# Kernel tuning notes

Measured on AMD Instinct MI355X. Metric: run time of the kernel, lower is better.

## Reference

```python
import jax, jax.numpy as jnp
import numpy as np

B, S, HID = 2, 2048, 3072
NH, NKV, HD = 16, 8, 256
N_REP = NH // NKV
BITS, BLK = 4, 128
THETA = 10000.0
NEG = -1e9


def quantize_bfp(x, bits=BITS, block_size=BLK):
    """Block-floating-point quantization: blocks of `block_size` along the last
    (head_dim) axis share one power-of-two exponent; mantissas get `bits` levels
    (sign + bits-1), round-to-nearest."""
    shape = x.shape
    xb = x.reshape(-1, block_size)
    maxabs = jnp.max(jnp.abs(xb), axis=-1, keepdims=True)
    e = jnp.floor(jnp.log2(jnp.maximum(maxabs, 1e-30)))
    scale = jnp.exp2(e - (bits - 2))  # largest mantissa ~ 2^(bits-1)-1 covers maxabs
    qmax = 2.0 ** (bits - 1) - 1.0
    q = jnp.clip(jnp.round(xb / scale), -qmax, qmax) * scale
    q = jnp.where(maxabs > 0, q, 0.0)
    return q.reshape(shape)


def rotate_half(x):
    x1, x2 = jnp.split(x, 2, axis=-1)
    return jnp.concatenate((-x2, x1), axis=-1)


def setup_inputs() -> dict:
    key = jax.random.key(0)
    ks = jax.random.split(key, 5)
    hidden_states = jax.random.normal(ks[0], (B, S, HID), dtype=jnp.float32)
    sd = 0.02
    Wq = jax.random.normal(ks[1], (NH * HD, HID), dtype=jnp.float32) * sd
    Wk = jax.random.normal(ks[2], (NKV * HD, HID), dtype=jnp.float32) * sd
    Wv = jax.random.normal(ks[3], (NKV * HD, HID), dtype=jnp.float32) * sd
    Wo = jax.random.normal(ks[4], (HID, NH * HD), dtype=jnp.float32) * sd
    # rotary tables (HF convention: concat(freqs, freqs))
    pos = jnp.arange(S, dtype=jnp.float32)
    inv_freq = 1.0 / (THETA ** (jnp.arange(0, HD, 2, dtype=jnp.float32) / HD))
    freqs = jnp.einsum('s,d->sd', pos, inv_freq)
    emb = jnp.concatenate((freqs, freqs), axis=-1)  # (S, HD)
    cos = jnp.cos(emb)[None]  # (1, S, HD)
    sin = jnp.sin(emb)[None]
    # additive causal mask (B, 1, S, S)
    causal = jnp.where(jnp.tril(jnp.ones((S, S), dtype=bool)), 0.0, NEG).astype(jnp.float32)
    attention_mask = jnp.broadcast_to(causal[None, None], (B, 1, S, S))
    return {"hidden_states": hidden_states, "Wq": Wq, "Wk": Wk, "Wv": Wv,
            "Wo": Wo, "cos": cos, "sin": sin, "attention_mask": attention_mask}


def reference(hidden_states, Wq, Wk, Wv, Wo, cos, sin, attention_mask):
    b, s, _ = hidden_states.shape
    q = jnp.einsum('bsh,dh->bsd', hidden_states, Wq).reshape(b, s, NH, HD).transpose(0, 2, 1, 3)
    k = jnp.einsum('bsh,dh->bsd', hidden_states, Wk).reshape(b, s, NKV, HD).transpose(0, 2, 1, 3)
    v = jnp.einsum('bsh,dh->bsd', hidden_states, Wv).reshape(b, s, NKV, HD).transpose(0, 2, 1, 3)
    # RoPE (cos/sin unsqueezed at dim 1 -> (1,1,S,HD))
    c, sn = cos[:, None], sin[:, None]
    q = q * c + rotate_half(q) * sn
    k = k * c + rotate_half(k) * sn
    # int4 BFP quantization of keys (along rows of head_dim)
    k = quantize_bfp(k)
    # GQA: repeat kv heads
    k = jnp.repeat(k, N_REP, axis=1)
    v = jnp.repeat(v, N_REP, axis=1)
    scores = jnp.einsum('bhqd,bhkd->bhqk', q, k) / jnp.sqrt(jnp.float32(HD))
    scores = scores + attention_mask
    attn = jax.nn.softmax(scores.astype(jnp.float32), axis=-1).astype(q.dtype)
    out = jnp.einsum('bhqk,bhkd->bhqd', attn, v)
    out = out.transpose(0, 2, 1, 3).reshape(b, s, NH * HD)
    return jnp.einsum('bsd,hd->bsh', out, Wo)
```

## Files before the change

kernel.cpp:

```cpp
#include <hip/hip_runtime.h>
#include <math.h>

#define Bsz 2
#define Ssz 2048
#define HIDs 3072
#define NHs 16
#define NKVs 8
#define HDs 256

typedef _Float16 f16;
typedef _Float16 f16x8 __attribute__((ext_vector_type(8)));
typedef _Float16 f16x4 __attribute__((ext_vector_type(4)));
typedef float f32x4 __attribute__((ext_vector_type(4)));

__device__ __forceinline__ void async16(const f16* g, f16* l) {
    __builtin_amdgcn_global_load_lds(
        (const __attribute__((address_space(1))) void*)g,
        (__attribute__((address_space(3))) void*)l, 16, 0, 0);
}

__device__ __forceinline__ float row_max16(float v) {
    int t;
    t = __builtin_amdgcn_mov_dpp(__float_as_int(v), 0x121, 0xf, 0xf, false);
    v = fmaxf(v, __int_as_float(t));
    t = __builtin_amdgcn_mov_dpp(__float_as_int(v), 0x122, 0xf, 0xf, false);
    v = fmaxf(v, __int_as_float(t));
    t = __builtin_amdgcn_mov_dpp(__float_as_int(v), 0x124, 0xf, 0xf, false);
    v = fmaxf(v, __int_as_float(t));
    t = __builtin_amdgcn_mov_dpp(__float_as_int(v), 0x128, 0xf, 0xf, false);
    v = fmaxf(v, __int_as_float(t));
    return v;
}
__device__ __forceinline__ float row_sum16(float v) {
    int t;
    t = __builtin_amdgcn_mov_dpp(__float_as_int(v), 0x121, 0xf, 0xf, false);
    v = v + __int_as_float(t);
    t = __builtin_amdgcn_mov_dpp(__float_as_int(v), 0x122, 0xf, 0xf, false);
    v = v + __int_as_float(t);
    t = __builtin_amdgcn_mov_dpp(__float_as_int(v), 0x124, 0xf, 0xf, false);
    v = v + __int_as_float(t);
    t = __builtin_amdgcn_mov_dpp(__float_as_int(v), 0x128, 0xf, 0xf, false);
    v = v + __int_as_float(t);
    return v;
}

#define N4_HS  3145728
#define N4_WQ  3145728
#define N4_WK  1572864
#define N4_WV  1572864
#define N4_WO  3145728
#define N4_TOT (N4_HS + N4_WQ + N4_WK + N4_WV + N4_WO)

__global__ void cast_all_kernel(const float4* __restrict__ hs, const float4* __restrict__ wq,
                                const float4* __restrict__ wk, const float4* __restrict__ wv,
                                const float4* __restrict__ wo,
                                f16x4* __restrict__ hs_h, f16x4* __restrict__ wq_h,
                                f16x4* __restrict__ wk_h, f16x4* __restrict__ wv_h,
                                f16x4* __restrict__ wo_h) {
    int i = blockIdx.x * blockDim.x + threadIdx.x;
    const float4* src; f16x4* dst; int off;
    if (i < N4_HS)                       { src = hs; dst = hs_h; off = i; }
    else if (i < N4_HS + N4_WQ)          { src = wq; dst = wq_h; off = i - N4_HS; }
    else if (i < N4_HS + N4_WQ + N4_WK)  { src = wk; dst = wk_h; off = i - (N4_HS + N4_WQ); }
    else if (i < N4_TOT - N4_WO)         { src = wv; dst = wv_h; off = i - (N4_HS + N4_WQ + N4_WK); }
    else                                 { src = wo; dst = wo_h; off = i - (N4_TOT - N4_WO); }
    float4 v = src[off];
    f16x4 r;
    r[0] = (f16)v.x; r[1] = (f16)v.y; r[2] = (f16)v.z; r[3] = (f16)v.w;
    dst[off] = r;
}

__global__ __launch_bounds__(256) void gemm_nt_f16(
    const f16* __restrict__ A, const f16* __restrict__ Bm, float* __restrict__ C,
    int M, int N, int K)
{
    __shared__ __align__(16) f16 As[128 * 32];
    __shared__ __align__(16) f16 Bs[128 * 32];
    const int tid  = threadIdx.x;
    const int wave = tid >> 6, lane = tid & 63;
    const int l15  = lane & 15, quad = lane >> 4;
    const int m0 = blockIdx.y * 128, n0 = blockIdx.x * 128;
    const int wm = (wave >> 1) * 64, wn = (wave & 1) * 64;
    const int srow = wave * 32 + (lane >> 2);
    const int scol = (lane & 3) * 8;

    f32x4 acc[4][4];
    const f32x4 fz = {0.f, 0.f, 0.f, 0.f};
#pragma unroll
    for (int i = 0; i < 4; i++)
#pragma unroll
        for (int j = 0; j < 4; j++) acc[i][j] = fz;

    const f16* Ag0 = A  + (size_t)(m0 + srow) * K + scol;
    const f16* Ag1 = A  + (size_t)(m0 + srow + 16) * K + scol;
    const f16* Bg0 = Bm + (size_t)(n0 + srow) * K + scol;
    const f16* Bg1 = Bm + (size_t)(n0 + srow + 16) * K + scol;
    f16* Al0 = As + (wave * 32) * 32;
    f16* Al1 = As + (wave * 32 + 16) * 32;
    f16* Bl0 = Bs + (wave * 32) * 32;
    f16* Bl1 = Bs + (wave * 32 + 16) * 32;

    for (int k0 = 0; k0 < K; k0 += 32) {
        __syncthreads();
        async16(Ag0 + k0, Al0);
        async16(Ag1 + k0, Al1);
        async16(Bg0 + k0, Bl0);
        async16(Bg1 + k0, Bl1);
        __syncthreads();
        f16x8 af[4], bfr[4];
#pragma unroll
        for (int i = 0; i < 4; i++)
            af[i] = *(const f16x8*)(As + (wm + i * 16 + l15) * 32 + quad * 8);
#pragma unroll
        for (int j = 0; j < 4; j++)
            bfr[j] = *(const f16x8*)(Bs + (wn + j * 16 + l15) * 32 + quad * 8);
#pragma unroll
        for (int i = 0; i < 4; i++)
#pragma unroll
            for (int j = 0; j < 4; j++)
                acc[i][j] = __builtin_amdgcn_mfma_f32_16x16x32_f16(af[i], bfr[j], acc[i][j], 0, 0, 0);
    }
#pragma unroll
    for (int i = 0; i < 4; i++) {
        const int r = m0 + wm + i * 16 + quad * 4;
#pragma unroll
        for (int j = 0; j < 4; j++) {
            const int c = n0 + wn + j * 16 + l15;
#pragma unroll
            for (int rr = 0; rr < 4; rr++)
                C[(size_t)(r + rr) * N + c] = acc[i][j][rr];
        }
    }
}

__global__ void rope_q_kernel(const float* __restrict__ qp, const float* __restrict__ cosb,
                              const float* __restrict__ sinb, f16* __restrict__ qo) {
    const int s = blockIdx.x, h = blockIdx.y, b = blockIdx.z;
    const int d = threadIdx.x;
    const float* row = qp + (size_t)(b * Ssz + s) * (NHs * HDs) + h * HDs;
    float x = row[d];
    float other = (d < 128) ? -row[d + 128] : row[d - 128];
    float val = (x * cosb[s * HDs + d] + other * sinb[s * HDs + d]) * 0.0625f;
    qo[((size_t)(b * NHs + h) * Ssz + s) * HDs + d] = (f16)val;
}

__global__ void rope_quant_k_kernel(const float* __restrict__ kp, const float* __restrict__ cosb,
                                    const float* __restrict__ sinb, f16* __restrict__ ko) {
    const int s = blockIdx.x, h = blockIdx.y, b = blockIdx.z;
    const int d = threadIdx.x;
    const float* row = kp + (size_t)(b * Ssz + s) * (NKVs * HDs) + h * HDs;
    float x = row[d];
    float other = (d < 128) ? -row[d + 128] : row[d - 128];
    float val = x * cosb[s * HDs + d] + other * sinb[s * HDs + d];
    __shared__ float red[256];
    red[d] = fabsf(val);
    __syncthreads();
    for (int off = 64; off >= 1; off >>= 1) {
        if ((d & 127) < off) red[d] = fmaxf(red[d], red[d + off]);
        __syncthreads();
    }
    float maxabs = red[d & 128];
    float out;
    if (maxabs > 0.f) {
        int ex;
        frexpf(maxabs, &ex);
        float scale = ldexpf(1.0f, ex - 3);
        float q = rintf(val / scale);
        q = fminf(7.f, fmaxf(-7.f, q));
        out = q * scale;
    } else out = 0.f;
    ko[((size_t)(b * NKVs + h) * Ssz + s) * HDs + d] = (f16)out;
}

__global__ __launch_bounds__(256) void transpose_v_kernel(
    const float* __restrict__ proj, f16* __restrict__ vt)
{
    const int s0 = blockIdx.x * 64, c0 = blockIdx.y * 64, b = blockIdx.z;
    const int tid = threadIdx.x;
    __shared__ f16 T[64 * 72];
    {
        const int r = tid >> 2, cc = (tid & 3) * 16;
        const float* src = proj + (size_t)(b * Ssz + s0 + r) * (NKVs * HDs) + c0 + cc;
        f16 tmp[16];
#pragma unroll
        for (int q4 = 0; q4 < 4; q4++) {
            float4 v = *(const float4*)(src + q4 * 4);
            tmp[q4 * 4 + 0] = (f16)v.x; tmp[q4 * 4 + 1] = (f16)v.y;
            tmp[q4 * 4 + 2] = (f16)v.z; tmp[q4 * 4 + 3] = (f16)v.w;
        }
        *(f16x8*)(T + r * 72 + cc)     = *(f16x8*)(tmp);
        *(f16x8*)(T + r * 72 + cc + 8) = *(f16x8*)(tmp + 8);
    }
    __syncthreads();
    {
        const int d = tid >> 2, sc = (tid & 3) * 16;
        f16 tmp[16];
#pragma unroll
        for (int j = 0; j < 16; j++) tmp[j] = T[(sc + j) * 72 + d];
        const int col = c0 + d;
        const int kh = col >> 8, dd = col & 255;
        f16* dst = vt + ((size_t)(b * NKVs + kh) * HDs + dd) * Ssz + s0 + sc;
        *(f16x8*)(dst)     = *(f16x8*)(tmp);
        *(f16x8*)(dst + 8) = *(f16x8*)(tmp + 8);
    }
}

__global__ __launch_bounds__(256, 2) void attn_kernel(
    const f16* __restrict__ Q,
    const f16* __restrict__ Kq,
    const f16* __restrict__ Vt,
    f16* __restrict__ O)
{
    const int qt = (gridDim.x - 1) - blockIdx.x;
    const int h = blockIdx.y, b = blockIdx.z;
    const int kh = h >> 1;
    const int tid = threadIdx.x;
    const int wave = tid >> 6, lane = tid & 63;
    const int l15 = lane & 15, quad = lane >> 4;
    const int wrow = qt * 128 + wave * 32;

    const f16* Qb  = Q  + ((size_t)(b * NHs  + h)  * Ssz) * HDs;
    const f16* Kg  = Kq + ((size_t)(b * NKVs + kh) * Ssz) * HDs;
    const f16* Vtg = Vt + ((size_t)(b * NKVs + kh) * HDs) * Ssz;

    __shared__ __align__(16) f16 Ks[2][32 * 256];
    __shared__ __align__(16) f16 Vs[2][256 * 32];
    __shared__ __align__(16) f16 Pl[4 * 32 * 40];
    f16* Pw = Pl + wave * 32 * 40;

    const int k_r  = lane >> 5;
    const int k_c  = lane & 31;
    const int v_r  = lane >> 2;
    const int v_gc = (lane & 3) ^ ((v_r >> 1) & 3);

    auto stage = [&](int kt2, int bb) {
        const int kvb_ = kt2 * 32;
#pragma unroll
        for (int t = 0; t < 4; t++) {
            const int r2 = wave * 8 + t * 2;
            const int gc = k_c ^ ((2 * t + k_r) & 7);
            async16(Kg + (size_t)(kvb_ + r2 + k_r) * 256 + gc * 8, &Ks[bb][r2 * 256]);
        }
#pragma unroll
        for (int t = 0; t < 4; t++) {
            const int d0 = wave * 64 + t * 16;
            async16(Vtg + (size_t)(d0 + v_r) * Ssz + kvb_ + v_gc * 8, &Vs[bb][d0 * 32]);
        }
    };

    f16x8 qf0[8], qf1[8];
    {
        const f16* qrow0 = Qb + (size_t)(wrow + l15) * HDs + quad * 8;
        const f16* qrow1 = qrow0 + (size_t)16 * HDs;
#pragma unroll
        for (int ks = 0; ks < 8; ks++) {
            qf0[ks] = *(const f16x8*)(qrow0 + ks * 32);
            qf1[ks] = *(const f16x8*)(qrow1 + ks * 32);
        }
    }

    const f32x4 fz = {0.f, 0.f, 0.f, 0.f};
    f32x4 accO0[16], accO1[16];
#pragma unroll
    for (int jn = 0; jn < 16; jn++) { accO0[jn] = fz; accO1[jn] = fz; }
    float mrow0[4], mrow1[4], lp0[4], lp1[4];
#pragma unroll
    for (int r = 0; r < 4; r++) { mrow0[r] = -1e30f; mrow1[r] = -1e30f; lp0[r] = 0.f; lp1[r] = 0.f; }

    const int nk = 4 * qt + 4;
    const int wave_max_row = wrow + 31;
    const int kswz = l15 & 7;
    const int vswz = (l15 >> 1) & 3;

    stage(0, 0);
    __syncthreads();

    for (int kt = 0; kt < nk; kt++) {
        const int kvb = kt * 32;
        const int cur = kt & 1;
        if (kt + 1 < nk) stage(kt + 1, cur ^ 1);
        const f16* Ksc = Ks[cur];
        const f16* Vsc = Vs[cur];

        if (kvb <= wave_max_row) {
            f32x4 s00 = fz, s01 = fz, s10 = fz, s11 = fz;
#pragma unroll
            for (int ks = 0; ks < 8; ks++) {
                const int cpos = ((ks * 4 + quad) ^ kswz) * 8;
                f16x8 kf0 = *(const f16x8*)(Ksc + l15 * 256 + cpos);
                f16x8 kf1 = *(const f16x8*)(Ksc + (16 + l15) * 256 + cpos);
                s00 = __builtin_amdgcn_mfma_f32_16x16x32_f16(qf0[ks], kf0, s00, 0, 0, 0);
                s01 = __builtin_amdgcn_mfma_f32_16x16x32_f16(qf0[ks], kf1, s01, 0, 0, 0);
                s10 = __builtin_amdgcn_mfma_f32_16x16x32_f16(qf1[ks], kf0, s10, 0, 0, 0);
                s11 = __builtin_amdgcn_mfma_f32_16x16x32_f16(qf1[ks], kf1, s11, 0, 0, 0);
            }
            float a0[4], a1[4];
            bool need = false;
            const bool diag = (kvb + 31 > wrow);
#pragma unroll
            for (int r = 0; r < 4; r++) {
                float x0 = s00[r], x1 = s01[r];
                const int row0 = wrow + quad * 4 + r;
                if (diag) {
                    if (kvb + l15 > row0)      x0 = -1e30f;
                    if (kvb + 16 + l15 > row0) x1 = -1e30f;
                }
                float rmax = row_max16(fmaxf(x0, x1));
                float mold = mrow0[r];
                bool upd = rmax > mold + 8.f;
                float mnew = upd ? rmax : mold;
                a0[r] = upd ? __expf(mold - rmax) : 1.0f;
                need = need || upd;
                float p0 = __expf(x0 - mnew);
                float p1 = __expf(x1 - mnew);
                lp0[r] = lp0[r] * a0[r] + (p0 + p1);
                mrow0[r] = mnew;
                Pw[(quad * 4 + r) * 40 + l15]      = (f16)p0;
                Pw[(quad * 4 + r) * 40 + 16 + l15] = (f16)p1;
                float y0 = s10[r], y1 = s11[r];
                const int row1 = row0 + 16;
                if (diag) {
                    if (kvb + l15 > row1)      y0 = -1e30f;
                    if (kvb + 16 + l15 > row1) y1 = -1e30f;
                }
                float rmax1 = row_max16(fmaxf(y0, y1));
                float mold1 = mrow1[r];
                bool upd1 = rmax1 > mold1 + 8.f;
                float mnew1 = upd1 ? rmax1 : mold1;
                a1[r] = upd1 ? __expf(mold1 - rmax1) : 1.0f;
                need = need || upd1;
                float q0 = __expf(y0 - mnew1);
                float q1 = __expf(y1 - mnew1);
                lp1[r] = lp1[r] * a1[r] + (q0 + q1);
                mrow1[r] = mnew1;
                Pw[(16 + quad * 4 + r) * 40 + l15]      = (f16)q0;
                Pw[(16 + quad * 4 + r) * 40 + 16 + l15] = (f16)q1;
            }
            if (__any(need)) {
#pragma unroll
                for (int jn = 0; jn < 16; jn++) {
                    f32x4 t0 = accO0[jn], t1 = accO1[jn];
                    t0[0] *= a0[0]; t0[1] *= a0[1]; t0[2] *= a0[2]; t0[3] *= a0[3];
                    t1[0] *= a1[0]; t1[1] *= a1[1]; t1[2] *= a1[2]; t1[3] *= a1[3];
                    accO0[jn] = t0; accO1[jn] = t1;
                }
            }
            f16x8 pf0 = *(const f16x8*)(Pw + l15 * 40 + quad * 8);
            f16x8 pf1 = *(const f16x8*)(Pw + (16 + l15) * 40 + quad * 8);
#pragma unroll
            for (int jn = 0; jn < 16; jn++) {
                f16x8 vf = *(const f16x8*)(Vsc + (jn * 16 + l15) * 32 + (quad ^ vswz) * 8);
                accO0[jn] = __builtin_amdgcn_mfma_f32_16x16x32_f16(pf0, vf, accO0[jn], 0, 0, 0);
                accO1[jn] = __builtin_amdgcn_mfma_f32_16x16x32_f16(pf1, vf, accO1[jn], 0, 0, 0);
            }
        }
        __syncthreads();
    }
#pragma unroll
    for (int r = 0; r < 4; r++) {
        const int row0 = wrow + quad * 4 + r;
        const float inv0 = 1.0f / row_sum16(lp0[r]);
        f16* orow0 = O + ((size_t)(b * Ssz) + row0) * (NHs * HDs) + h * HDs;
#pragma unroll
        for (int jn = 0; jn < 16; jn++)
            orow0[jn * 16 + l15] = (f16)(accO0[jn][r] * inv0);
        const int row1 = row0 + 16;
        const float inv1 = 1.0f / row_sum16(lp1[r]);
        f16* orow1 = O + ((size_t)(b * Ssz) + row1) * (NHs * HDs) + h * HDs;
#pragma unroll
        for (int jn = 0; jn < 16; jn++)
            orow1[jn * 16 + l15] = (f16)(accO1[jn][r] * inv1);
    }
}

extern "C" void kernel_launch(void* const* d_in, const int* in_sizes, int n_in,
                              void* d_out, int out_size, void* d_ws, size_t ws_size,
                              hipStream_t stream) {
    const float* hs   = (const float*)d_in[0];
    const float* Wq   = (const float*)d_in[1];
    const float* Wk   = (const float*)d_in[2];
    const float* Wv   = (const float*)d_in[3];
    const float* Wo   = (const float*)d_in[4];
    const float* cosb = (const float*)d_in[5];
    const float* sinb = (const float*)d_in[6];
    float* out = (float*)d_out;

    char* ws = (char*)d_ws;
    f16*   hs_h = (f16*)(ws);
    f16*   wo_h = (f16*)(ws + 25165824);
    float* proj = (float*)(ws + 50331648);
    f16*   q_h  = (f16*)(ws + 117440512);
    f16*   k_h  = (f16*)(ws + 150994944);
    f16*   vt_h = (f16*)(ws + 167772160);
    f16*   ao_h = (f16*)proj;

    cast_all_kernel<<<N4_TOT / 256, 256, 0, stream>>>(
        (const float4*)hs, (const float4*)Wq, (const float4*)Wk,
        (const float4*)Wv, (const float4*)Wo,
        (f16x4*)hs_h, (f16x4*)q_h, (f16x4*)k_h, (f16x4*)vt_h, (f16x4*)wo_h);

    gemm_nt_f16<<<dim3(4096 / 128, 4096 / 128), 256, 0, stream>>>(hs_h, q_h, proj, 4096, 4096, 3072);
    rope_q_kernel<<<dim3(Ssz, NHs, Bsz), 256, 0, stream>>>(proj, cosb, sinb, q_h);
    gemm_nt_f16<<<dim3(2048 / 128, 4096 / 128), 256, 0, stream>>>(hs_h, k_h, proj, 4096, 2048, 3072);
    rope_quant_k_kernel<<<dim3(Ssz, NKVs, Bsz), 256, 0, stream>>>(proj, cosb, sinb, k_h);
    gemm_nt_f16<<<dim3(2048 / 128, 4096 / 128), 256, 0, stream>>>(hs_h, vt_h, proj, 4096, 2048, 3072);
    transpose_v_kernel<<<dim3(Ssz / 64, (NKVs * HDs) / 64, Bsz), 256, 0, stream>>>(proj, vt_h);
    attn_kernel<<<dim3(Ssz / 128, NHs, Bsz), 256, 0, stream>>>(q_h, k_h, vt_h, ao_h);
    gemm_nt_f16<<<dim3(3072 / 128, 4096 / 128), 256, 0, stream>>>(ao_h, wo_h, out, 4096, 3072, 4096);
}
```

Before: 1.085 ms.

## Remap attention blocks to XCDs for KV-head L2 locality and single-buffer K/V

Block indices are remapped so that all query tiles sharing one (batch, KV head) pair land on the same XCD, with causal tiles ordered to balance load, aiming to improve L2 reuse of K and V. The double-buffered K/V LDS staging is also replaced by a single buffer loaded synchronously each iteration. This halves LDS use, which may allow more blocks per CU, but it exposes global-load latency because loads no longer overlap compute. The remapping hard-codes the grid shape (16x16x2).

```diff
diff --git a/kernel.cpp b/kernel.cpp
--- a/kernel.cpp
+++ b/kernel.cpp
@@ -211,9 +211,18 @@
     const f16* __restrict__ Vt,
     f16* __restrict__ O)
 {
-    const int qt = (gridDim.x - 1) - blockIdx.x;
-    const int h = blockIdx.y, b = blockIdx.z;
-    const int kh = h >> 1;
+    const int flat = blockIdx.x + (blockIdx.y << 4) + (blockIdx.z << 8);
+    const int xcd  = flat & 7;
+    const int slot = flat >> 3;
+    const int psel = slot >> 5;
+    const int pair = (xcd << 1) | psel;
+    const int b    = pair >> 3;
+    const int kh   = pair & 7;
+    const int sub  = slot & 31;
+    const int h    = (kh << 1) | (sub >> 4);
+    const int qt_raw = sub & 15;
+    const int qt   = psel ? qt_raw : (15 - qt_raw);
+
     const int tid = threadIdx.x;
     const int wave = tid >> 6, lane = tid & 63;
     const int l15 = lane & 15, quad = lane >> 4;
@@ -223,8 +232,8 @@
     const f16* Kg  = Kq + ((size_t)(b * NKVs + kh) * Ssz) * HDs;
     const f16* Vtg = Vt + ((size_t)(b * NKVs + kh) * HDs) * Ssz;
 
-    __shared__ __align__(16) f16 Ks[2][32 * 256];
-    __shared__ __align__(16) f16 Vs[2][256 * 32];
+    __shared__ __align__(16) f16 Ks[32 * 256];
+    __shared__ __align__(16) f16 Vs[256 * 32];
     __shared__ __align__(16) f16 Pl[4 * 32 * 40];
     f16* Pw = Pl + wave * 32 * 40;
 
@@ -233,21 +242,6 @@
     const int v_r  = lane >> 2;
     const int v_gc = (lane & 3) ^ ((v_r >> 1) & 3);
 
-    auto stage = [&](int kt2, int bb) {
-        const int kvb_ = kt2 * 32;
-#pragma unroll
-        for (int t = 0; t < 4; t++) {
-            const int r2 = wave * 8 + t * 2;
-            const int gc = k_c ^ ((2 * t + k_r) & 7);
-            async16(Kg + (size_t)(kvb_ + r2 + k_r) * 256 + gc * 8, &Ks[bb][r2 * 256]);
-        }
-#pragma unroll
-        for (int t = 0; t < 4; t++) {
-            const int d0 = wave * 64 + t * 16;
-            async16(Vtg + (size_t)(d0 + v_r) * Ssz + kvb_ + v_gc * 8, &Vs[bb][d0 * 32]);
-        }
-    };
-
     f16x8 qf0[8], qf1[8];
     {
         const f16* qrow0 = Qb + (size_t)(wrow + l15) * HDs + quad * 8;
@@ -272,23 +266,29 @@
     const int kswz = l15 & 7;
     const int vswz = (l15 >> 1) & 3;
 
-    stage(0, 0);
-    __syncthreads();
-
     for (int kt = 0; kt < nk; kt++) {
         const int kvb = kt * 32;
-        const int cur = kt & 1;
-        if (kt + 1 < nk) stage(kt + 1, cur ^ 1);
-        const f16* Ksc = Ks[cur];
-        const f16* Vsc = Vs[cur];
+        __syncthreads();
+#pragma unroll
+        for (int t = 0; t < 4; t++) {
+            const int r2 = wave * 8 + t * 2;
+            const int gc = k_c ^ ((2 * t + k_r) & 7);
+            async16(Kg + (size_t)(kvb + r2 + k_r) * 256 + gc * 8, Ks + r2 * 256);
+        }
+#pragma unroll
+        for (int t = 0; t < 4; t++) {
+            const int d0 = wave * 64 + t * 16;
+            async16(Vtg + (size_t)(d0 + v_r) * Ssz + kvb + v_gc * 8, Vs + d0 * 32);
+        }
+        __syncthreads();
 
         if (kvb <= wave_max_row) {
             f32x4 s00 = fz, s01 = fz, s10 = fz, s11 = fz;
 #pragma unroll
             for (int ks = 0; ks < 8; ks++) {
                 const int cpos = ((ks * 4 + quad) ^ kswz) * 8;
-                f16x8 kf0 = *(const f16x8*)(Ksc + l15 * 256 + cpos);
-                f16x8 kf1 = *(const f16x8*)(Ksc + (16 + l15) * 256 + cpos);
+                f16x8 kf0 = *(const f16x8*)(Ks + l15 * 256 + cpos);
+                f16x8 kf1 = *(const f16x8*)(Ks + (16 + l15) * 256 + cpos);
                 s00 = __builtin_amdgcn_mfma_f32_16x16x32_f16(qf0[ks], kf0, s00, 0, 0, 0);
                 s01 = __builtin_amdgcn_mfma_f32_16x16x32_f16(qf0[ks], kf1, s01, 0, 0, 0);
                 s10 = __builtin_amdgcn_mfma_f32_16x16x32_f16(qf1[ks], kf0, s10, 0, 0, 0);
@@ -349,12 +349,11 @@
             f16x8 pf1 = *(const f16x8*)(Pw + (16 + l15) * 40 + quad * 8);
 #pragma unroll
             for (int jn = 0; jn < 16; jn++) {
-                f16x8 vf = *(const f16x8*)(Vsc + (jn * 16 + l15) * 32 + (quad ^ vswz) * 8);
+                f16x8 vf = *(const f16x8*)(Vs + (jn * 16 + l15) * 32 + (quad ^ vswz) * 8);
                 accO0[jn] = __builtin_amdgcn_mfma_f32_16x16x32_f16(pf0, vf, accO0[jn], 0, 0, 0);
                 accO1[jn] = __builtin_amdgcn_mfma_f32_16x16x32_f16(pf1, vf, accO1[jn], 0, 0, 0);
             }
         }
-        __syncthreads();
     }
 #pragma unroll
     for (int r = 0; r < 4; r++) {
```

Result: faster. 970.7 us (-10.6%).
